# Kernel optimization log

Hardware: AMD Instinct MI355X
Metric: run time of the kernel (lower is better)

Reference implementation:

```python
import jax, jax.numpy as jnp
import numpy as np

B, H, W = 16, 256, 256
C = 64          # width
M1, M2 = 12, 12 # retained Fourier modes
FC_HID = 128


def setup_inputs() -> dict:
    key = jax.random.key(0)
    ks = jax.random.split(key, 10)
    scale = 1.0 / (C * C)
    inp = {
        "x": jax.random.normal(ks[0], (B, H, W, 1), dtype=jnp.float32),
        "fc0_w": jax.random.normal(ks[1], (1, C), dtype=jnp.float32) * (1.0 / np.sqrt(1)),
        "fc0_b": jnp.zeros((C,), dtype=jnp.float32),
        # 4 layers x {weights1, weights2} x [Cin, Cout, M1, M2] x {re, im}
        "sc_w": jax.random.uniform(ks[2], (4, 2, C, C, M1, M2, 2), dtype=jnp.float32) * scale,
        # 1x1 conv weights [layer, Cout, Cin] and biases [layer, Cout]
        "pw_w": jax.random.normal(ks[3], (4, C, C), dtype=jnp.float32) * (1.0 / np.sqrt(C)),
        "pw_b": jnp.zeros((4, C), dtype=jnp.float32),
        "fc1_w": jax.random.normal(ks[4], (C, FC_HID), dtype=jnp.float32) * (1.0 / np.sqrt(C)),
        "fc1_b": jnp.zeros((FC_HID,), dtype=jnp.float32),
        "fc2_w": jax.random.normal(ks[5], (FC_HID, 1), dtype=jnp.float32) * (1.0 / np.sqrt(FC_HID)),
        "fc2_b": jnp.zeros((1,), dtype=jnp.float32),
    }
    return inp


def _spectral_conv(x, w1, w2):
    # x: [B, C, H, W] real; w1, w2: [Cin, Cout, M1, M2] complex
    xf = jnp.fft.rfft2(x, axes=(-2, -1))                # [B, C, H, W//2+1]
    top = jnp.einsum('bixy,ioxy->boxy', xf[:, :, :M1, :M2], w1)
    bot = jnp.einsum('bixy,ioxy->boxy', xf[:, :, -M1:, :M2], w2)
    out_ft = jnp.zeros((x.shape[0], w1.shape[1], x.shape[2], x.shape[3] // 2 + 1),
                       dtype=jnp.complex64)
    out_ft = out_ft.at[:, :, :M1, :M2].set(top)
    out_ft = out_ft.at[:, :, -M1:, :M2].set(bot)
    return jnp.fft.irfft2(out_ft, s=(x.shape[2], x.shape[3]), axes=(-2, -1))


def _gelu(x):
    return jax.nn.gelu(x, approximate=False)  # torch F.gelu default = exact erf


def reference(x, fc0_w, fc0_b, sc_w, pw_w, pw_b, fc1_w, fc1_b, fc2_w, fc2_b):
    # lift: [B,H,W,1] -> [B,H,W,C] -> [B,C,H,W]
    h = jnp.einsum('bhwi,ic->bhwc', x, fc0_w) + fc0_b
    h = jnp.transpose(h, (0, 3, 1, 2))
    scw = sc_w[..., 0] + 1j * sc_w[..., 1]  # [4, 2, C, C, M1, M2] complex
    for l in range(4):
        x1 = _spectral_conv(h, scw[l, 0], scw[l, 1])
        x2 = jnp.einsum('bihw,oi->bohw', h, pw_w[l]) + pw_b[l][None, :, None, None]
        h = x1 + x2
        if l < 3:
            h = _gelu(h)
    h = jnp.transpose(h, (0, 2, 3, 1))  # [B,H,W,C]
    h = _gelu(jnp.einsum('bhwc,cd->bhwd', h, fc1_w) + fc1_b)
    out = jnp.einsum('bhwd,do->bhwo', h, fc2_w) + fc2_b
    return out
```

## Files before the change

### kernel.cpp

```cpp
#include <hip/hip_runtime.h>
#include <hip/hip_bf16.h>
#include <math.h>

#define Hn 256
#define Wn 256
#define Cn 64
#define Mk 12
#define NM 24
#define FCH 128
#define HW 65536

using half8 = __attribute__((ext_vector_type(8))) _Float16;
using f32x4 = __attribute__((ext_vector_type(4))) float;

__device__ __forceinline__ float gelu_exact(float x) {
    return 0.5f * x * (1.0f + erff(x * 0.7071067811865476f));
}
__device__ __forceinline__ unsigned short f2h(float f) {
    _Float16 h = (_Float16)f;
    return __builtin_bit_cast(unsigned short, h);
}

__global__ __launch_bounds__(256) void k_init_tables(float* tc, float* ts,
                                                     float* twc, float* tws,
                                                     float* tcs,
                                                     unsigned short* bfr,
                                                     unsigned short* tfr,
                                                     unsigned short* yfrA) {
    int i = threadIdx.x;
    const float step = 0.024543692606170259f;
    float c = cosf(i * step), s = sinf(i * step);
    tc[i] = c; ts[i] = s;
    tcs[2 * i] = c; tcs[2 * i + 1] = s;
    for (int k = 0; k < Mk; ++k) {
        int idx = (i * k) & 255;
        twc[i * Mk + k] = cosf(idx * step);
        tws[i * Mk + k] = sinf(idx * step);
    }
    for (int e = i; e < 8192; e += 256) {
        int j  = e & 7;
        int l  = (e >> 3) & 63;
        int sn = e >> 9;
        int col = (sn & 1) * 16 + (l & 15);
        int ky = col >> 1, p = col & 1;
        int k  = (sn >> 1) * 32 + ((l >> 4) & 3) * 8 + j;
        int idx = (ky * k) & 255;
        float v = p ? -sinf(idx * step) : cosf(idx * step);
        bfr[e] = f2h(v);
    }
    for (int e = i; e < 12288; e += 256) {
        int j  = e & 7;
        int l  = (e >> 3) & 63;
        int sm = e >> 9;
        int mt = sm % 3, s2 = sm / 3;
        int r  = mt * 16 + (l & 15);
        int hh = s2 * 32 + ((l >> 4) & 3) * 8 + j;
        int m  = (r < 24) ? r : (r - 24);
        int kx = (m < Mk) ? m : (232 + m);
        int idx = (kx * hh) & 255;
        float v = (r < 24) ? cosf(idx * step) : sinf(idx * step);
        tfr[e] = f2h(v);
    }
    for (int e = i; e < 16384; e += 256) {
        int j  = e & 7;
        int l  = (e >> 3) & 63;
        int sm = e >> 9;
        int mt = sm & 15, s2 = sm >> 4;
        int hh = mt * 16 + (l & 15);
        int k  = s2 * 32 + ((l >> 4) & 3) * 8 + j;
        int m = k >> 1, sgn = k & 1;
        float v = 0.f;
        if (m < 24) {
            int kx = (m < Mk) ? m : (232 + m);
            int idx = (kx * hh) & 255;
            v = sgn ? sinf(idx * step) : cosf(idx * step);
        }
        yfrA[e] = f2h(v);
    }
}

__global__ __launch_bounds__(256) void k_prep_frag(const float* __restrict__ pww,
                                                   const float* __restrict__ fc1w,
                                                   unsigned short* __restrict__ efr,
                                                   unsigned short* __restrict__ pwfr,
                                                   unsigned short* __restrict__ fc1fr) {
    int e = blockIdx.x * 256 + threadIdx.x;
    const float step = 0.024543692606170259f;
    int j = e & 7, l = (e >> 3) & 63;
    int row = l & 15;
    int k = ((l >> 4) & 3) * 8 + j;
    if (e < 8192) {
        int mt = (e >> 9) & 15;
        int pix = mt * 16 + row;
        float v = 0.f;
        if (k < 12) v = cosf(((k * pix) & 255) * step);
        else if (k < 24) v = -sinf((((k - 12) * pix) & 255) * step);
        efr[e] = f2h(v);
    } else if (e < 24576) {
        int e2 = e - 8192;
        int nt = (e2 >> 9) & 3;
        int ks = (e2 >> 11) & 1;
        int l4 = e2 >> 12;
        int o = nt * 16 + row;
        int i = ks * 32 + k;
        pwfr[e2] = f2h(pww[(size_t)(l4 * 64 + o) * 64 + i]);
    } else {
        int e2 = e - 24576;
        int nt = (e2 >> 9) & 7;
        int ks = (e2 >> 12) & 1;
        int d = nt * 16 + row;
        int i = ks * 32 + k;
        fc1fr[e2] = f2h(fc1w[i * 128 + d]);
    }
}

__global__ __launch_bounds__(256) void k_prep_wfrag(const float* __restrict__ scw,
                                                    unsigned short* __restrict__ wfr) {
    __shared__ float Ws[8192];
    int mat = blockIdx.x;
    int lj = mat / 144, kxw = (mat / 12) % 12, ky = mat % 12;
    int t = threadIdx.x;
    const float* base = scw + (((size_t)lj * 4096) * 144 + kxw * 12 + ky) * 2;
#pragma unroll
    for (int r = 0; r < 16; ++r) {
        int idx = r * 256 + t;
        float2 v = *(const float2*)(base + (size_t)idx * 288);
        Ws[idx * 2] = v.x; Ws[idx * 2 + 1] = v.y;
    }
    __syncthreads();
    unsigned short* dst = wfr + (size_t)mat * 16384;
#pragma unroll
    for (int u = 0; u < 8; ++u) {
        int lin = u * 256 + t;
        int lane = lin & 63, nt = (lin >> 6) & 7, s = lin >> 9;
        int col = nt * 16 + (lane & 15);
        int o = col >> 1, pp = col & 1;
        int tg = (lane >> 4) & 3;
        unsigned pk[4];
#pragma unroll
        for (int jp = 0; jp < 4; ++jp) {
            unsigned short hv[2];
#pragma unroll
            for (int hz = 0; hz < 2; ++hz) {
                int k = s * 32 + tg * 8 + jp * 2 + hz;
                int i = k >> 1, p = k & 1;
                float wr_ = Ws[(i * 64 + o) * 2];
                float wi_ = Ws[(i * 64 + o) * 2 + 1];
                float v = (p == 0) ? (pp == 0 ? wr_ : wi_)
                                   : (pp == 0 ? -wi_ : wr_);
                hv[hz] = f2h(v);
            }
            pk[jp] = hv[0] | ((unsigned)hv[1] << 16);
        }
        uint4 w4 = {pk[0], pk[1], pk[2], pk[3]};
        *(uint4*)(dst + lin * 8) = w4;
    }
}

__global__ __launch_bounds__(64) void k_dftw_x(const float* __restrict__ x,
                                               float* __restrict__ Xxw,
                                               const float* __restrict__ twc,
                                               const float* __restrict__ tws) {
    int r = blockIdx.x * 64 + threadIdx.x;
    const float* hp = x + (size_t)r * Wn;
    float xr[Mk], xi[Mk];
#pragma unroll
    for (int k = 0; k < Mk; ++k) { xr[k] = 0.f; xi[k] = 0.f; }
    for (int w4 = 0; w4 < 64; ++w4) {
        float4 v = ((const float4*)hp)[w4];
        float vv[4] = {v.x, v.y, v.z, v.w};
#pragma unroll
        for (int j = 0; j < 4; ++j) {
            int wbase = (w4 * 4 + j) * Mk;
#pragma unroll
            for (int k = 0; k < Mk; ++k) {
                xr[k] += vv[j] * twc[wbase + k];
                xi[k] -= vv[j] * tws[wbase + k];
            }
        }
    }
    float* op = Xxw + (size_t)r * (2 * Mk);
#pragma unroll
    for (int k = 0; k < Mk; ++k) { op[2 * k] = xr[k]; op[2 * k + 1] = xi[k]; }
}

__global__ __launch_bounds__(256) void k_xdfth(const float* __restrict__ Xxw,
                                               float* __restrict__ Xfx,
                                               const float* __restrict__ tc,
                                               const float* __restrict__ ts) {
    int t = blockIdx.x * 256 + threadIdx.x;
    if (t >= 16 * 288) return;
    int ky = t % Mk;
    int m  = (t / Mk) % NM;
    int b  = t / 288;
    int kx = (m < Mk) ? m : (232 + m);
    const float* base = Xxw + (size_t)b * Hn * 2 * Mk + 2 * ky;
    float ar = 0.f, ai = 0.f;
    for (int hh = 0; hh < Hn; ++hh) {
        float vr = base[hh * 2 * Mk];
        float vi = base[hh * 2 * Mk + 1];
        int idx = (kx * hh) & 255;
        float c = tc[idx], s = ts[idx];
        ar += vr * c + vi * s;
        ai += vi * c - vr * s;
    }
    Xfx[2 * t] = ar;
    Xfx[2 * t + 1] = ai;
}

__global__ __launch_bounds__(256) void k_mixZ2(const float* __restrict__ xin,
                                               const unsigned short* __restrict__ wfr,
                                               const float* __restrict__ w0,
                                               const float* __restrict__ b0v,
                                               float* __restrict__ Z,
                                               int l, int first, int b0, int bc) {
    __shared__ __align__(16) char smem[4096];
    int t = threadIdx.x;
    int lane = t & 63, q = t >> 6, tg = (lane >> 4) & 3;
    int blk2 = blockIdx.x;
    int hlf = blk2 & 1;
    int blk = blk2 >> 1;
    int jj = blk / 144, kxw = (blk / 12) % 12, ky = blk % 12;
    int mm = jj * 12 + kxw;
    int mk = mm * 12 + ky;
    int mat = (l * 2 + jj) * 144 + kxw * 12 + ky;
    {
        int b = t >> 4, c16 = t & 15;
        uint4 pk = {0u, 0u, 0u, 0u};
        if (b < bc) {
            if (first) {
                float xr = xin[((b0 + b) * 288 + mk) * 2] * 0.0625f;
                float xi = xin[((b0 + b) * 288 + mk) * 2 + 1] * 0.0625f;
                float4 wv = *(const float4*)(w0 + c16 * 4);
                float4 bv = {0.f, 0.f, 0.f, 0.f};
                if (mk == 0) {
                    float4 bb = *(const float4*)(b0v + c16 * 4);
                    bv.x = 4096.f * bb.x; bv.y = 4096.f * bb.y;
                    bv.z = 4096.f * bb.z; bv.w = 4096.f * bb.w;
                }
                pk.x = f2h(wv.x * xr + bv.x) | ((unsigned)f2h(wv.x * xi) << 16);
                pk.y = f2h(wv.y * xr + bv.y) | ((unsigned)f2h(wv.y * xi) << 16);
                pk.z = f2h(wv.z * xr + bv.z) | ((unsigned)f2h(wv.z * xi) << 16);
                pk.w = f2h(wv.w * xr + bv.w) | ((unsigned)f2h(wv.w * xi) << 16);
            } else {
                const float* src = xin + ((size_t)b * 288 + mk) * 128 + c16 * 8;
                float4 v0 = *(const float4*)(src);
                float4 v1 = *(const float4*)(src + 4);
                pk.x = f2h(v0.x * 0.0625f) | ((unsigned)f2h(v0.y * 0.0625f) << 16);
                pk.y = f2h(v0.z * 0.0625f) | ((unsigned)f2h(v0.w * 0.0625f) << 16);
                pk.z = f2h(v1.x * 0.0625f) | ((unsigned)f2h(v1.y * 0.0625f) << 16);
                pk.w = f2h(v1.z * 0.0625f) | ((unsigned)f2h(v1.w * 0.0625f) << 16);
            }
        }
        *(uint4*)(smem + ((b * 256 + c16 * 16) ^ ((b & 7) << 4))) = pk;
    }
    __syncthreads();
    int nt = hlf * 4 + q;
    const uint4* bt = (const uint4*)wfr + (size_t)mat * 2048;
    f32x4 ac = {0.f, 0.f, 0.f, 0.f};
    int brow = lane & 15;
#pragma unroll
    for (int s = 0; s < 4; ++s) {
        half8 af = *(const half8*)(smem + ((brow * 256 + s * 64 + tg * 16) ^ ((brow & 7) << 4)));
        half8 bf = __builtin_bit_cast(half8, bt[(s * 8 + nt) * 64 + lane]);
        ac = __builtin_amdgcn_mfma_f32_16x16x32_f16(af, bf, ac, 0, 0, 0);
    }
    const float sc = 16.0f * 2.0f / 65536.0f;
    int col = nt * 16 + (lane & 15);
    int o = col >> 1, pp = col & 1;
#pragma unroll
    for (int r = 0; r < 4; ++r) {
        int bb = (lane >> 4) * 4 + r;
        if (bb < bc)
            Z[(((size_t)bb * 12 + ky) * 64 + o) * 48 + mm * 2 + pp] = ac[r] * sc;
    }
}

__global__ __launch_bounds__(256) void k_prepY(const float* __restrict__ Z,
                                               const unsigned short* __restrict__ yfrA,
                                               unsigned short* __restrict__ Ybuf) {
    __shared__ __align__(16) unsigned short bf[8192];
    int blkb = blockIdx.x / 12, ky = blockIdx.x % 12;
    int t = threadIdx.x;
    int lane = t & 63, q = t >> 6;
    const float* Zbb = Z + ((size_t)blkb * 12 + ky) * 3072;
#pragma unroll
    for (int u4 = 0; u4 < 4; ++u4) {
        int lin = u4 * 256 + t;
        int lane_ = lin & 63, nt_ = (lin >> 6) & 7, s_ = lin >> 9;
        int tg_ = (lane_ >> 4) & 3;
        int col = nt_ * 16 + (lane_ & 15);
        int o = col >> 1, sy = col & 1;
        int kbase = s_ * 32 + tg_ * 8;
        uint4 pk = {0u, 0u, 0u, 0u};
        if (kbase < 48) {
            const float* zp = Zbb + o * 48 + kbase;
            float4 z0 = *(const float4*)zp;
            float4 z1 = *(const float4*)(zp + 4);
            float zv[8] = {z0.x, z0.y, z0.z, z0.w, z1.x, z1.y, z1.z, z1.w};
            unsigned pv[4];
#pragma unroll
            for (int jp = 0; jp < 4; ++jp) {
                float v0, v1;
                if (sy == 0) { v0 = zv[2 * jp];     v1 = -zv[2 * jp + 1]; }
                else         { v0 = zv[2 * jp + 1]; v1 = zv[2 * jp]; }
                pv[jp] = f2h(v0) | ((unsigned)f2h(v1) << 16);
            }
            pk.x = pv[0]; pk.y = pv[1]; pk.z = pv[2]; pk.w = pv[3];
        }
        *(uint4*)(bf + lin * 8) = pk;
    }
    __syncthreads();
    const uint4* A4 = (const uint4*)yfrA;
    const uint4* B4 = (const uint4*)bf;
    unsigned short* Yb = Ybuf + (size_t)blkb * 524288;
    float dcs = (ky == 0) ? 0.5f : 1.0f;
#pragma unroll
    for (int mtl = 0; mtl < 4; ++mtl) {
        int mt = q * 4 + mtl;
        half8 a0 = __builtin_bit_cast(half8, A4[(0 * 16 + mt) * 64 + lane]);
        half8 a1 = __builtin_bit_cast(half8, A4[(1 * 16 + mt) * 64 + lane]);
#pragma unroll
        for (int nt_ = 0; nt_ < 8; ++nt_) {
            f32x4 acc = {0.f, 0.f, 0.f, 0.f};
            acc = __builtin_amdgcn_mfma_f32_16x16x32_f16(a0,
                    __builtin_bit_cast(half8, B4[(0 * 8 + nt_) * 64 + lane]), acc, 0, 0, 0);
            acc = __builtin_amdgcn_mfma_f32_16x16x32_f16(a1,
                    __builtin_bit_cast(half8, B4[(1 * 8 + nt_) * 64 + lane]), acc, 0, 0, 0);
            int col = nt_ * 16 + (lane & 15);
            int o = col >> 1, sy = col & 1;
            int u = ky + 12 * sy;
            float sc2 = (sy == 0) ? dcs : 1.0f;
            int rbase = mt * 16 + (lane >> 4) * 4;
#pragma unroll
            for (int r = 0; r < 4; ++r)
                Yb[((size_t)(rbase + r) * 64 + o) * 32 + u] = f2h(acc[r] * sc2);
        }
    }
    if (ky == 0) {
        uint4 z4 = {0u, 0u, 0u, 0u};
        for (int e = t; e < 16384; e += 256)
            *(uint4*)(Yb + (size_t)e * 32 + 24) = z4;
    }
}

__global__ __launch_bounds__(256) void k_dfth(const unsigned short* __restrict__ Xw,
                                              float* __restrict__ Xf2,
                                              const unsigned short* __restrict__ tfr) {
    __shared__ __align__(16) char smem[65536];
    int b = blockIdx.x / 12, ky = blockIdx.x % 12;
    int t = threadIdx.x;
    int lane = t & 63, q = t >> 6;
    const unsigned short* Pre = Xw + ((size_t)b * 24 + ky * 2) * 16384;
    const unsigned short* Pim = Pre + 16384;
    int c = lane;
#pragma unroll 4
    for (int k = 0; k < 32; ++k) {
        int hh0 = k * 8 + q * 2;
        unsigned r0 = Pre[hh0 * 64 + c], r1 = Pre[(hh0 + 1) * 64 + c];
        unsigned i0 = Pim[hh0 * 64 + c], i1 = Pim[(hh0 + 1) * 64 + c];
        unsigned u0 = r0 | (r1 << 16);
        unsigned u1 = i0 | (i1 << 16);
        int ch0 = 2 * c, ch1 = 2 * c + 1;
        *(unsigned int*)(smem + ch0 * 512 + ((2 * hh0) ^ ((ch0 & 7) << 4))) = u0;
        *(unsigned int*)(smem + ch1 * 512 + ((2 * hh0) ^ ((ch1 & 7) << 4))) = u1;
    }
    __syncthreads();
    int ct0 = q * 2;
    int tg = (lane >> 4) & 3;
    f32x4 a00 = {0,0,0,0}, a01 = {0,0,0,0}, a10 = {0,0,0,0};
    f32x4 a11 = {0,0,0,0}, a20 = {0,0,0,0}, a21 = {0,0,0,0};
    const uint4* tf4 = (const uint4*)tfr;
#pragma unroll
    for (int s = 0; s < 8; ++s) {
        half8 af0 = __builtin_bit_cast(half8, tf4[(s * 3 + 0) * 64 + lane]);
        half8 af1 = __builtin_bit_cast(half8, tf4[(s * 3 + 1) * 64 + lane]);
        half8 af2 = __builtin_bit_cast(half8, tf4[(s * 3 + 2) * 64 + lane]);
        int chan0 = ct0 * 16 + (lane & 15);
        int chan1 = chan0 + 16;
        int off = s * 64 + tg * 16;
        half8 b0 = *(const half8*)(smem + chan0 * 512 + (off ^ ((chan0 & 7) << 4)));
        half8 b1 = *(const half8*)(smem + chan1 * 512 + (off ^ ((chan1 & 7) << 4)));
        a00 = __builtin_amdgcn_mfma_f32_16x16x32_f16(af0, b0, a00, 0, 0, 0);
        a01 = __builtin_amdgcn_mfma_f32_16x16x32_f16(af0, b1, a01, 0, 0, 0);
        a10 = __builtin_amdgcn_mfma_f32_16x16x32_f16(af1, b0, a10, 0, 0, 0);
        a11 = __builtin_amdgcn_mfma_f32_16x16x32_f16(af1, b1, a11, 0, 0, 0);
        a20 = __builtin_amdgcn_mfma_f32_16x16x32_f16(af2, b0, a20, 0, 0, 0);
        a21 = __builtin_amdgcn_mfma_f32_16x16x32_f16(af2, b1, a21, 0, 0, 0);
    }
    __syncthreads();
    float* Cs = (float*)smem;
    {
        int rl = (lane >> 4) * 4;
        int chan0 = ct0 * 16 + (lane & 15);
#pragma unroll
        for (int r = 0; r < 4; ++r) {
            Cs[(0  + rl + r) * 128 + chan0]      = a00[r];
            Cs[(0  + rl + r) * 128 + chan0 + 16] = a01[r];
            Cs[(16 + rl + r) * 128 + chan0]      = a10[r];
            Cs[(16 + rl + r) * 128 + chan0 + 16] = a11[r];
            Cs[(32 + rl + r) * 128 + chan0]      = a20[r];
            Cs[(32 + rl + r) * 128 + chan0 + 16] = a21[r];
        }
    }
    __syncthreads();
#pragma unroll
    for (int k = 0; k < 6; ++k) {
        int p = t + 256 * k;
        int m = p >> 6, i = p & 63;
        float r1 = Cs[m * 128 + 2 * i];
        float i1 = Cs[m * 128 + 2 * i + 1];
        float r2 = Cs[(24 + m) * 128 + 2 * i];
        float i2 = Cs[(24 + m) * 128 + 2 * i + 1];
        ((float2*)Xf2)[((size_t)b * 288 + m * 12 + ky) * 64 + i] =
            make_float2((r1 + i2) * 16.0f, (i1 - r2) * 16.0f);
    }
}

__global__ __launch_bounds__(256, 4) void k_fusedA(const float* __restrict__ x0,
        const unsigned short* hin, const unsigned short* __restrict__ Ybuf,
        const float* __restrict__ pwb,
        const float* __restrict__ w0, const float* __restrict__ b0v,
        unsigned short* hout, unsigned short* __restrict__ XwOut,
        const unsigned short* __restrict__ bfr,
        const unsigned short* __restrict__ efr,
        const unsigned short* __restrict__ pwfr,
        int l, int first) {
    __shared__ __align__(16) char smem[32768];
    int b  = blockIdx.x >> 8;
    int hh = blockIdx.x & 255;
    int w  = threadIdx.x;
    int lane = w & 63, q = w >> 6;
    int tg = (lane >> 4) & 3;
    {
        int swz = (w & 7) << 4;
        if (first) {
            float xv = x0[(size_t)b * HW + hh * 256 + w];
#pragma unroll
            for (int ic = 0; ic < 4; ++ic) {
                unsigned pv[8];
#pragma unroll
                for (int j2 = 0; j2 < 16; j2 += 2) {
                    float a0 = w0[ic * 16 + j2] * xv + b0v[ic * 16 + j2];
                    float a1 = w0[ic * 16 + j2 + 1] * xv + b0v[ic * 16 + j2 + 1];
                    pv[j2 >> 1] = f2h(a0) | ((unsigned)f2h(a1) << 16);
                }
                uint4 lo = {pv[0], pv[1], pv[2], pv[3]};
                uint4 hi = {pv[4], pv[5], pv[6], pv[7]};
                *(uint4*)(smem + ((w * 128 + ic * 32) ^ swz)) = lo;
                *(uint4*)(smem + ((w * 128 + ic * 32 + 16) ^ swz)) = hi;
            }
        } else {
            const unsigned short* hb = hin + (size_t)b * Cn * HW + hh * 256 + w;
#pragma unroll
            for (int ic = 0; ic < 4; ++ic) {
                unsigned pv[8];
#pragma unroll
                for (int j2 = 0; j2 < 16; j2 += 2) {
                    unsigned a0 = hb[(size_t)(ic * 16 + j2) * HW];
                    unsigned a1 = hb[(size_t)(ic * 16 + j2 + 1) * HW];
                    pv[j2 >> 1] = a0 | (a1 << 16);
                }
                uint4 lo = {pv[0], pv[1], pv[2], pv[3]};
                uint4 hi = {pv[4], pv[5], pv[6], pv[7]};
                *(uint4*)(smem + ((w * 128 + ic * 32) ^ swz)) = lo;
                *(uint4*)(smem + ((w * 128 + ic * 32 + 16) ^ swz)) = hi;
            }
        }
    }
    __syncthreads();
    uint2 gp[4][4];
    {
        const uint4* efr4 = (const uint4*)efr;
        const uint4* pw4  = (const uint4*)pwfr;
        const uint4* Y4 = (const uint4*)Ybuf + ((size_t)b * 256 + hh) * 256;
        float biasn[4];
        half8 ybf[4]; uint4 cwa[4], cwb[4];
#pragma unroll
        for (int nt = 0; nt < 4; ++nt) {
            int o = nt * 16 + (lane & 15);
            biasn[nt] = pwb[l * 64 + o];
            ybf[nt] = __builtin_bit_cast(half8, Y4[o * 4 + tg]);
            cwa[nt] = pw4[((l * 2 + 0) * 4 + nt) * 64 + lane];
            cwb[nt] = pw4[((l * 2 + 1) * 4 + nt) * 64 + lane];
        }
#pragma unroll
        for (int mt = 0; mt < 4; ++mt) {
            int mtA = q * 4 + mt;
            half8 ea = __builtin_bit_cast(half8, efr4[mtA * 64 + lane]);
            int row = mtA * 16 + (lane & 15);
            int rsw = (row & 7) << 4;
            half8 a0 = *(const half8*)(smem + ((row * 128 + tg * 16) ^ rsw));
            half8 a1 = *(const half8*)(smem + ((row * 128 + 64 + tg * 16) ^ rsw));
#pragma unroll
            for (int nt = 0; nt < 4; ++nt) {
                f32x4 acc = {0.f, 0.f, 0.f, 0.f};
                acc = __builtin_amdgcn_mfma_f32_16x16x32_f16(ea, ybf[nt], acc, 0, 0, 0);
                acc = __builtin_amdgcn_mfma_f32_16x16x32_f16(a0, __builtin_bit_cast(half8, cwa[nt]), acc, 0, 0, 0);
                acc = __builtin_amdgcn_mfma_f32_16x16x32_f16(a1, __builtin_bit_cast(half8, cwb[nt]), acc, 0, 0, 0);
                float g0 = gelu_exact(acc[0] + biasn[nt]);
                float g1 = gelu_exact(acc[1] + biasn[nt]);
                float g2 = gelu_exact(acc[2] + biasn[nt]);
                float g3 = gelu_exact(acc[3] + biasn[nt]);
                gp[mt][nt].x = f2h(g0) | ((unsigned)f2h(g1) << 16);
                gp[mt][nt].y = f2h(g2) | ((unsigned)f2h(g3) << 16);
            }
        }
    }
    unsigned short* hnb = hout + (size_t)b * Cn * HW + hh * 256;
#pragma unroll
    for (int mt = 0; mt < 4; ++mt) {
        int pbase = (q * 4 + mt) * 16 + (lane >> 4) * 4;
#pragma unroll
        for (int nt = 0; nt < 4; ++nt) {
            int o = nt * 16 + (lane & 15);
            *(uint2*)(hnb + (size_t)o * HW + pbase) = gp[mt][nt];
        }
    }
    __syncthreads();
#pragma unroll
    for (int mt = 0; mt < 4; ++mt) {
        int pbase = (q * 4 + mt) * 16 + (lane >> 4) * 4;
#pragma unroll
        for (int nt = 0; nt < 4; ++nt) {
            int o = nt * 16 + (lane & 15);
            int sidx = (((pbase >> 3) ^ (o & 7)) << 3) | (pbase & 7);
            *(uint2*)(smem + o * 512 + sidx * 2) = gp[mt][nt];
        }
    }
    __syncthreads();
    {
        int arow = q * 16 + (lane & 15);
        const uint4* bt = (const uint4*)bfr;
        f32x4 ac0 = {0.f, 0.f, 0.f, 0.f};
        f32x4 ac1 = {0.f, 0.f, 0.f, 0.f};
#pragma unroll
        for (int s = 0; s < 8; ++s) {
            int abyte = (arow * 512 + s * 64 + tg * 16) ^ ((arow & 7) << 4);
            half8 af = __builtin_bit_cast(half8, *(const uint4*)(smem + abyte));
            half8 b0 = __builtin_bit_cast(half8, bt[(s * 2 + 0) * 64 + lane]);
            half8 b1 = __builtin_bit_cast(half8, bt[(s * 2 + 1) * 64 + lane]);
            ac0 = __builtin_amdgcn_mfma_f32_16x16x32_f16(af, b0, ac0, 0, 0, 0);
            ac1 = __builtin_amdgcn_mfma_f32_16x16x32_f16(af, b1, ac1, 0, 0, 0);
        }
        unsigned short* Xwb = XwOut + (size_t)b * 393216;
        int rbase = q * 16 + (lane >> 4) * 4;
#pragma unroll
        for (int n = 0; n < 2; ++n) {
            f32x4 ac = n ? ac1 : ac0;
            int col = n * 16 + (lane & 15);
            int ky = col >> 1, p = col & 1;
            if (ky < Mk) {
                uint2 pk;
                pk.x = f2h(ac[0] * 0.0625f) | ((unsigned)f2h(ac[1] * 0.0625f) << 16);
                pk.y = f2h(ac[2] * 0.0625f) | ((unsigned)f2h(ac[3] * 0.0625f) << 16);
                *(uint2*)(Xwb + ((size_t)(ky * 2 + p) * 256 + hh) * 64 + rbase) = pk;
            }
        }
    }
}

__global__ __launch_bounds__(256, 4) void k_fusedB(const unsigned short* __restrict__ hin,
        const unsigned short* __restrict__ Ybuf, const float* __restrict__ pwb,
        const float* __restrict__ fc1b, const float* __restrict__ fc2w,
        const float* __restrict__ fc2b, float* __restrict__ outp,
        const unsigned short* __restrict__ efr,
        const unsigned short* __restrict__ pwfr,
        const unsigned short* __restrict__ fc1fr) {
    __shared__ __align__(16) char smem[32768];
    int b  = blockIdx.x >> 8;
    int hh = blockIdx.x & 255;
    int w  = threadIdx.x;
    int lane = w & 63, q = w >> 6;
    int tg = (lane >> 4) & 3;
    {
        int swz = (w & 7) << 4;
        const unsigned short* hb = hin + (size_t)b * Cn * HW + hh * 256 + w;
#pragma unroll
        for (int ic = 0; ic < 4; ++ic) {
            unsigned pv[8];
#pragma unroll
            for (int j2 = 0; j2 < 16; j2 += 2) {
                unsigned a0 = hb[(size_t)(ic * 16 + j2) * HW];
                unsigned a1 = hb[(size_t)(ic * 16 + j2 + 1) * HW];
                pv[j2 >> 1] = a0 | (a1 << 16);
            }
            uint4 lo = {pv[0], pv[1], pv[2], pv[3]};
            uint4 hi = {pv[4], pv[5], pv[6], pv[7]};
            *(uint4*)(smem + ((w * 128 + ic * 32) ^ swz)) = lo;
            *(uint4*)(smem + ((w * 128 + ic * 32 + 16) ^ swz)) = hi;
        }
    }
    __syncthreads();
    uint2 R2[16];
    {
        const uint4* efr4 = (const uint4*)efr;
        const uint4* pw4 = (const uint4*)pwfr;
        const uint4* Y4 = (const uint4*)Ybuf + ((size_t)b * 256 + hh) * 256;
        half8 ay  = __builtin_bit_cast(half8, Y4[(q * 16 + (lane & 15)) * 4 + tg]);
        half8 aw0 = __builtin_bit_cast(half8, pw4[((3 * 2 + 0) * 4 + q) * 64 + lane]);
        half8 aw1 = __builtin_bit_cast(half8, pw4[((3 * 2 + 1) * 4 + q) * 64 + lane]);
        int obase = q * 16 + (lane >> 4) * 4;
        float4 bias4 = *(const float4*)(pwb + 3 * 64 + obase);
#pragma unroll
        for (int nt = 0; nt < 16; ++nt) {
            half8 eb = __builtin_bit_cast(half8, efr4[nt * 64 + lane]);
            int pix = nt * 16 + (lane & 15);
            int psw = (pix & 7) << 4;
            half8 b0 = *(const half8*)(smem + ((pix * 128 + tg * 16) ^ psw));
            half8 b1 = *(const half8*)(smem + ((pix * 128 + 64 + tg * 16) ^ psw));
            f32x4 acc = {0.f, 0.f, 0.f, 0.f};
            acc = __builtin_amdgcn_mfma_f32_16x16x32_f16(ay, eb, acc, 0, 0, 0);
            acc = __builtin_amdgcn_mfma_f32_16x16x32_f16(aw0, b0, acc, 0, 0, 0);
            acc = __builtin_amdgcn_mfma_f32_16x16x32_f16(aw1, b1, acc, 0, 0, 0);
            R2[nt].x = f2h(acc[0] + bias4.x) | ((unsigned)f2h(acc[1] + bias4.y) << 16);
            R2[nt].y = f2h(acc[2] + bias4.z) | ((unsigned)f2h(acc[3] + bias4.w) << 16);
        }
    }
    __syncthreads();
    {
        int obase = q * 16 + (lane >> 4) * 4;
#pragma unroll
        for (int nt = 0; nt < 16; ++nt) {
            int pix = nt * 16 + (lane & 15);
            *(uint2*)(smem + ((pix * 128 + obase * 2) ^ ((pix & 7) << 4))) = R2[nt];
        }
    }
    __syncthreads();
    const uint4* f14 = (const uint4*)fc1fr;
    float w2v[8], fb1[8];
#pragma unroll
    for (int nt = 0; nt < 8; ++nt) {
        w2v[nt] = fc2w[nt * 16 + (lane & 15)];
        fb1[nt] = fc1b[nt * 16 + (lane & 15)];
    }
    float fb = fc2b[0];
    float* ob = outp + (size_t)b * HW + hh * 256;
#pragma unroll
    for (int mt = 0; mt < 4; ++mt) {
        int mtA = q * 4 + mt;
        int row = mtA * 16 + (lane & 15);
        int rsw = (row & 7) << 4;
        half8 a0 = *(const half8*)(smem + ((row * 128 + tg * 16) ^ rsw));
        half8 a1 = *(const half8*)(smem + ((row * 128 + 64 + tg * 16) ^ rsw));
        float s0 = 0.f, s1 = 0.f, s2 = 0.f, s3 = 0.f;
#pragma unroll
        for (int nt = 0; nt < 8; ++nt) {
            f32x4 acc = {0.f, 0.f, 0.f, 0.f};
            acc = __builtin_amdgcn_mfma_f32_16x16x32_f16(a0, __builtin_bit_cast(half8, f14[(0 * 8 + nt) * 64 + lane]), acc, 0, 0, 0);
            acc = __builtin_amdgcn_mfma_f32_16x16x32_f16(a1, __builtin_bit_cast(half8, f14[(1 * 8 + nt) * 64 + lane]), acc, 0, 0, 0);
            s0 += gelu_exact(acc[0] + fb1[nt]) * w2v[nt];
            s1 += gelu_exact(acc[1] + fb1[nt]) * w2v[nt];
            s2 += gelu_exact(acc[2] + fb1[nt]) * w2v[nt];
            s3 += gelu_exact(acc[3] + fb1[nt]) * w2v[nt];
        }
#pragma unroll
        for (int msk = 1; msk <= 8; msk <<= 1) {
            s0 += __shfl_xor(s0, msk);
            s1 += __shfl_xor(s1, msk);
            s2 += __shfl_xor(s2, msk);
            s3 += __shfl_xor(s3, msk);
        }
        int cc = lane & 15;
        if (cc < 4) {
            float v = (cc == 0) ? s0 : (cc == 1) ? s1 : (cc == 2) ? s2 : s3;
            ob[mtA * 16 + (lane >> 4) * 4 + cc] = v + fb;
        }
    }
}

extern "C" void kernel_launch(void* const* d_in, const int* in_sizes, int n_in,
                              void* d_out, int out_size, void* d_ws, size_t ws_size,
                              hipStream_t stream) {
    const float* x    = (const float*)d_in[0];
    const float* fc0w = (const float*)d_in[1];
    const float* fc0b = (const float*)d_in[2];
    const float* scw  = (const float*)d_in[3];
    const float* pww  = (const float*)d_in[4];
    const float* pwb  = (const float*)d_in[5];
    const float* fc1w = (const float*)d_in[6];
    const float* fc1b = (const float*)d_in[7];
    const float* fc2w = (const float*)d_in[8];
    const float* fc2b = (const float*)d_in[9];
    float* out = (float*)d_out;
    float* ws  = (float*)d_ws;

    const size_t basef = 9586688;
    const size_t perbf = 2629632;
    int bc = 0;
    for (int cand = 16; cand >= 1; cand >>= 1)
        if ((basef + perbf * (size_t)cand) * 4 <= ws_size) { bc = cand; break; }
    if (bc == 0) return;

    float* tabc = ws;
    float* tabs = tabc + 256;
    float* twc  = tabs + 256;
    float* tws_ = twc + 3072;
    float* tcs  = tws_ + 3072;
    float* bfr  = tcs + 512;
    float* tfr  = bfr + 4096;
    float* yfrA = tfr + 6144;
    float* efr  = yfrA + 8192;
    float* pwfr = efr + 4096;
    float* fc1f = pwfr + 8192;
    float* Xfx  = fc1f + 4096;
    float* wfr  = Xfx + 9216;
    float* Xxw  = wfr + 9437184;
    float* hbuf = ws + basef;
    unsigned short* h16  = (unsigned short*)hbuf;
    unsigned short* Xw16 = (unsigned short*)(hbuf + (size_t)bc * 2097152);
    float* Zb   = hbuf + (size_t)bc * (2097152 + 196608);
    float* Xf2  = Zb + (size_t)bc * 36864;
    unsigned short* Ybuf = (unsigned short*)(Xf2 + (size_t)bc * 36864);

    k_init_tables<<<1, 256, 0, stream>>>(tabc, tabs, twc, tws_, tcs,
                                         (unsigned short*)bfr,
                                         (unsigned short*)tfr,
                                         (unsigned short*)yfrA);
    k_prep_frag<<<128, 256, 0, stream>>>(pww, fc1w,
                                         (unsigned short*)efr,
                                         (unsigned short*)pwfr,
                                         (unsigned short*)fc1f);
    k_prep_wfrag<<<1152, 256, 0, stream>>>(scw, (unsigned short*)wfr);
    k_dftw_x<<<64, 64, 0, stream>>>(x, Xxw, twc, tws_);
    k_xdfth<<<18, 256, 0, stream>>>(Xxw, Xfx, tabc, tabs);

    for (int b0 = 0; b0 < 16; b0 += bc) {
        k_mixZ2<<<576, 256, 0, stream>>>(Xfx, (const unsigned short*)wfr,
                                         fc0w, fc0b, Zb, 0, 1, b0, bc);
        k_prepY<<<bc * 12, 256, 0, stream>>>(Zb, (const unsigned short*)yfrA, Ybuf);
        k_fusedA<<<bc * 256, 256, 0, stream>>>(x + (size_t)b0 * HW, h16, Ybuf, pwb,
                                               fc0w, fc0b, h16, Xw16,
                                               (const unsigned short*)bfr,
                                               (const unsigned short*)efr,
                                               (const unsigned short*)pwfr, 0, 1);
        for (int l = 1; l <= 2; ++l) {
            k_dfth<<<bc * 12, 256, 0, stream>>>(Xw16, Xf2, (const unsigned short*)tfr);
            k_mixZ2<<<576, 256, 0, stream>>>(Xf2, (const unsigned short*)wfr,
                                             fc0w, fc0b, Zb, l, 0, b0, bc);
            k_prepY<<<bc * 12, 256, 0, stream>>>(Zb, (const unsigned short*)yfrA, Ybuf);
            k_fusedA<<<bc * 256, 256, 0, stream>>>(x, h16, Ybuf, pwb,
                                                   fc0w, fc0b, h16, Xw16,
                                                   (const unsigned short*)bfr,
                                                   (const unsigned short*)efr,
                                                   (const unsigned short*)pwfr, l, 0);
        }
        k_dfth<<<bc * 12, 256, 0, stream>>>(Xw16, Xf2, (const unsigned short*)tfr);
        k_mixZ2<<<576, 256, 0, stream>>>(Xf2, (const unsigned short*)wfr,
                                         fc0w, fc0b, Zb, 3, 0, b0, bc);
        k_prepY<<<bc * 12, 256, 0, stream>>>(Zb, (const unsigned short*)yfrA, Ybuf);
        k_fusedB<<<bc * 256, 256, 0, stream>>>(h16, Ybuf, pwb, fc1b, fc2w, fc2b,
                                               out + (size_t)b0 * HW,
                                               (const unsigned short*)efr,
                                               (const unsigned short*)pwfr,
                                               (const unsigned short*)fc1f);
    }
}
```

Before: 1.321 ms.

## Store spectral coefficients as fp16 and split fusedB into half-row blocks

k_dfth now writes its Fourier coefficients as packed fp16 instead of float2, folding the ×16 and ×1/16 scales together so they cancel. k_mixZ2 loads those fp16 values directly, which halves that intermediate buffer and drops the per-element conversion. Separately, k_fusedB now handles half a row (128 pixels) per block with 16KB of shared memory, launches twice as many blocks and raises the launch bound to allow 8 blocks per CU. This aims for more occupancy and parallelism in the final stage, at the cost of more blocks and repeated weight-fragment loads. The fp16 intermediate could lose some accuracy if coefficient magnitudes exceed fp16 range.

```diff
diff --git a/kernel.cpp b/kernel.cpp
--- a/kernel.cpp
+++ b/kernel.cpp
@@ -209,6 +209,7 @@
 }
 
 __global__ __launch_bounds__(256) void k_mixZ2(const float* __restrict__ xin,
+                                               const unsigned short* __restrict__ xin16,
                                                const unsigned short* __restrict__ wfr,
                                                const float* __restrict__ w0,
                                                const float* __restrict__ b0v,
@@ -243,13 +244,7 @@
                 pk.z = f2h(wv.z * xr + bv.z) | ((unsigned)f2h(wv.z * xi) << 16);
                 pk.w = f2h(wv.w * xr + bv.w) | ((unsigned)f2h(wv.w * xi) << 16);
             } else {
-                const float* src = xin + ((size_t)b * 288 + mk) * 128 + c16 * 8;
-                float4 v0 = *(const float4*)(src);
-                float4 v1 = *(const float4*)(src + 4);
-                pk.x = f2h(v0.x * 0.0625f) | ((unsigned)f2h(v0.y * 0.0625f) << 16);
-                pk.y = f2h(v0.z * 0.0625f) | ((unsigned)f2h(v0.w * 0.0625f) << 16);
-                pk.z = f2h(v1.x * 0.0625f) | ((unsigned)f2h(v1.y * 0.0625f) << 16);
-                pk.w = f2h(v1.z * 0.0625f) | ((unsigned)f2h(v1.w * 0.0625f) << 16);
+                pk = *(const uint4*)(xin16 + ((size_t)b * 288 + mk) * 128 + c16 * 8);
             }
         }
         *(uint4*)(smem + ((b * 256 + c16 * 16) ^ ((b & 7) << 4))) = pk;
@@ -345,7 +340,7 @@
 }
 
 __global__ __launch_bounds__(256) void k_dfth(const unsigned short* __restrict__ Xw,
-                                              float* __restrict__ Xf2,
+                                              unsigned short* __restrict__ Xf16,
                                               const unsigned short* __restrict__ tfr) {
     __shared__ __align__(16) char smem[65536];
     int b = blockIdx.x / 12, ky = blockIdx.x % 12;
@@ -412,8 +407,8 @@
         float i1 = Cs[m * 128 + 2 * i + 1];
         float r2 = Cs[(24 + m) * 128 + 2 * i];
         float i2 = Cs[(24 + m) * 128 + 2 * i + 1];
-        ((float2*)Xf2)[((size_t)b * 288 + m * 12 + ky) * 64 + i] =
-            make_float2((r1 + i2) * 16.0f, (i1 - r2) * 16.0f);
+        ((unsigned int*)Xf16)[((size_t)b * 288 + m * 12 + ky) * 64 + i] =
+            (unsigned)f2h(r1 + i2) | ((unsigned)f2h(i1 - r2) << 16);
     }
 }
 
@@ -560,24 +555,29 @@
     }
 }
 
-__global__ __launch_bounds__(256, 4) void k_fusedB(const unsigned short* __restrict__ hin,
+__global__ __launch_bounds__(256, 8) void k_fusedB(const unsigned short* __restrict__ hin,
         const unsigned short* __restrict__ Ybuf, const float* __restrict__ pwb,
         const float* __restrict__ fc1b, const float* __restrict__ fc2w,
         const float* __restrict__ fc2b, float* __restrict__ outp,
         const unsigned short* __restrict__ efr,
         const unsigned short* __restrict__ pwfr,
         const unsigned short* __restrict__ fc1fr) {
-    __shared__ __align__(16) char smem[32768];
-    int b  = blockIdx.x >> 8;
-    int hh = blockIdx.x & 255;
+    __shared__ __align__(16) char smem[16384];
+    int blk = blockIdx.x;
+    int b  = blk >> 9;
+    int hh = (blk >> 1) & 255;
+    int hf = blk & 1;
     int w  = threadIdx.x;
     int lane = w & 63, q = w >> 6;
     int tg = (lane >> 4) & 3;
     {
-        int swz = (w & 7) << 4;
-        const unsigned short* hb = hin + (size_t)b * Cn * HW + hh * 256 + w;
-#pragma unroll
-        for (int ic = 0; ic < 4; ++ic) {
+        int pix = w & 127;
+        int cg  = w >> 7;
+        int swz = (pix & 7) << 4;
+        const unsigned short* hb = hin + (size_t)b * Cn * HW + hh * 256 + hf * 128 + pix;
+#pragma unroll
+        for (int ic2 = 0; ic2 < 2; ++ic2) {
+            int ic = cg * 2 + ic2;
             unsigned pv[8];
 #pragma unroll
             for (int j2 = 0; j2 < 16; j2 += 2) {
@@ -587,12 +587,12 @@
             }
             uint4 lo = {pv[0], pv[1], pv[2], pv[3]};
             uint4 hi = {pv[4], pv[5], pv[6], pv[7]};
-            *(uint4*)(smem + ((w * 128 + ic * 32) ^ swz)) = lo;
-            *(uint4*)(smem + ((w * 128 + ic * 32 + 16) ^ swz)) = hi;
-        }
-    }
-    __syncthreads();
-    uint2 R2[16];
+            *(uint4*)(smem + ((pix * 128 + ic * 32) ^ swz)) = lo;
+            *(uint4*)(smem + ((pix * 128 + ic * 32 + 16) ^ swz)) = hi;
+        }
+    }
+    __syncthreads();
+    uint2 R2[8];
     {
         const uint4* efr4 = (const uint4*)efr;
         const uint4* pw4 = (const uint4*)pwfr;
@@ -603,12 +603,12 @@
         int obase = q * 16 + (lane >> 4) * 4;
         float4 bias4 = *(const float4*)(pwb + 3 * 64 + obase);
 #pragma unroll
-        for (int nt = 0; nt < 16; ++nt) {
-            half8 eb = __builtin_bit_cast(half8, efr4[nt * 64 + lane]);
-            int pix = nt * 16 + (lane & 15);
-            int psw = (pix & 7) << 4;
-            half8 b0 = *(const half8*)(smem + ((pix * 128 + tg * 16) ^ psw));
-            half8 b1 = *(const half8*)(smem + ((pix * 128 + 64 + tg * 16) ^ psw));
+        for (int nt = 0; nt < 8; ++nt) {
+            half8 eb = __builtin_bit_cast(half8, efr4[(hf * 8 + nt) * 64 + lane]);
+            int pixL = nt * 16 + (lane & 15);
+            int psw = (pixL & 7) << 4;
+            half8 b0 = *(const half8*)(smem + ((pixL * 128 + tg * 16) ^ psw));
+            half8 b1 = *(const half8*)(smem + ((pixL * 128 + 64 + tg * 16) ^ psw));
             f32x4 acc = {0.f, 0.f, 0.f, 0.f};
             acc = __builtin_amdgcn_mfma_f32_16x16x32_f16(ay, eb, acc, 0, 0, 0);
             acc = __builtin_amdgcn_mfma_f32_16x16x32_f16(aw0, b0, acc, 0, 0, 0);
@@ -621,9 +621,9 @@
     {
         int obase = q * 16 + (lane >> 4) * 4;
 #pragma unroll
-        for (int nt = 0; nt < 16; ++nt) {
-            int pix = nt * 16 + (lane & 15);
-            *(uint2*)(smem + ((pix * 128 + obase * 2) ^ ((pix & 7) << 4))) = R2[nt];
+        for (int nt = 0; nt < 8; ++nt) {
+            int pixL = nt * 16 + (lane & 15);
+            *(uint2*)(smem + ((pixL * 128 + obase * 2) ^ ((pixL & 7) << 4))) = R2[nt];
         }
     }
     __syncthreads();
@@ -635,11 +635,11 @@
         fb1[nt] = fc1b[nt * 16 + (lane & 15)];
     }
     float fb = fc2b[0];
-    float* ob = outp + (size_t)b * HW + hh * 256;
-#pragma unroll
-    for (int mt = 0; mt < 4; ++mt) {
-        int mtA = q * 4 + mt;
-        int row = mtA * 16 + (lane & 15);
+    float* ob = outp + (size_t)b * HW + hh * 256 + hf * 128;
+#pragma unroll
+    for (int mt = 0; mt < 2; ++mt) {
+        int mtL = q * 2 + mt;
+        int row = mtL * 16 + (lane & 15);
         int rsw = (row & 7) << 4;
         half8 a0 = *(const half8*)(smem + ((row * 128 + tg * 16) ^ rsw));
         half8 a1 = *(const half8*)(smem + ((row * 128 + 64 + tg * 16) ^ rsw));
@@ -664,7 +664,7 @@
         int cc = lane & 15;
         if (cc < 4) {
             float v = (cc == 0) ? s0 : (cc == 1) ? s1 : (cc == 2) ? s2 : s3;
-            ob[mtA * 16 + (lane >> 4) * 4 + cc] = v + fb;
+            ob[mtL * 16 + (lane >> 4) * 4 + cc] = v + fb;
         }
     }
 }
@@ -686,7 +686,7 @@
     float* ws  = (float*)d_ws;
 
     const size_t basef = 9586688;
-    const size_t perbf = 2629632;
+    const size_t perbf = 2611200;
     int bc = 0;
     for (int cand = 16; cand >= 1; cand >>= 1)
         if ((basef + perbf * (size_t)cand) * 4 <= ws_size) { bc = cand; break; }
@@ -710,8 +710,8 @@
     unsigned short* h16  = (unsigned short*)hbuf;
     unsigned short* Xw16 = (unsigned short*)(hbuf + (size_t)bc * 2097152);
     float* Zb   = hbuf + (size_t)bc * (2097152 + 196608);
-    float* Xf2  = Zb + (size_t)bc * 36864;
-    unsigned short* Ybuf = (unsigned short*)(Xf2 + (size_t)bc * 36864);
+    unsigned short* Xf16 = (unsigned short*)(Zb + (size_t)bc * 36864);
+    unsigned short* Ybuf = (unsigned short*)(Zb + (size_t)bc * (36864 + 18432));
 
     k_init_tables<<<1, 256, 0, stream>>>(tabc, tabs, twc, tws_, tcs,
                                          (unsigned short*)bfr,
@@ -726,7 +726,7 @@
     k_xdfth<<<18, 256, 0, stream>>>(Xxw, Xfx, tabc, tabs);
 
     for (int b0 = 0; b0 < 16; b0 += bc) {
-        k_mixZ2<<<576, 256, 0, stream>>>(Xfx, (const unsigned short*)wfr,
+        k_mixZ2<<<576, 256, 0, stream>>>(Xfx, Xf16, (const unsigned short*)wfr,
                                          fc0w, fc0b, Zb, 0, 1, b0, bc);
         k_prepY<<<bc * 12, 256, 0, stream>>>(Zb, (const unsigned short*)yfrA, Ybuf);
         k_fusedA<<<bc * 256, 256, 0, stream>>>(x + (size_t)b0 * HW, h16, Ybuf, pwb,
@@ -735,8 +735,8 @@
                                                (const unsigned short*)efr,
                                                (const unsigned short*)pwfr, 0, 1);
         for (int l = 1; l <= 2; ++l) {
-            k_dfth<<<bc * 12, 256, 0, stream>>>(Xw16, Xf2, (const unsigned short*)tfr);
-            k_mixZ2<<<576, 256, 0, stream>>>(Xf2, (const unsigned short*)wfr,
+            k_dfth<<<bc * 12, 256, 0, stream>>>(Xw16, Xf16, (const unsigned short*)tfr);
+            k_mixZ2<<<576, 256, 0, stream>>>(Xfx, Xf16, (const unsigned short*)wfr,
                                              fc0w, fc0b, Zb, l, 0, b0, bc);
             k_prepY<<<bc * 12, 256, 0, stream>>>(Zb, (const unsigned short*)yfrA, Ybuf);
             k_fusedA<<<bc * 256, 256, 0, stream>>>(x, h16, Ybuf, pwb,
@@ -745,11 +745,11 @@
                                                    (const unsigned short*)efr,
                                                    (const unsigned short*)pwfr, l, 0);
         }
-        k_dfth<<<bc * 12, 256, 0, stream>>>(Xw16, Xf2, (const unsigned short*)tfr);
-        k_mixZ2<<<576, 256, 0, stream>>>(Xf2, (const unsigned short*)wfr,
+        k_dfth<<<bc * 12, 256, 0, stream>>>(Xw16, Xf16, (const unsigned short*)tfr);
+        k_mixZ2<<<576, 256, 0, stream>>>(Xfx, Xf16, (const unsigned short*)wfr,
                                          fc0w, fc0b, Zb, 3, 0, b0, bc);
         k_prepY<<<bc * 12, 256, 0, stream>>>(Zb, (const unsigned short*)yfrA, Ybuf);
-        k_fusedB<<<bc * 256, 256, 0, stream>>>(h16, Ybuf, pwb, fc1b, fc2w, fc2b,
+        k_fusedB<<<bc * 512, 256, 0, stream>>>(h16, Ybuf, pwb, fc1b, fc2w, fc2b,
                                                out + (size_t)b0 * HW,
                                                (const unsigned short*)efr,
                                                (const unsigned short*)pwfr,
```

New measurement: 1.685 ms. +27.6%, slower.
